# Performance work log

Hardware: AMD Instinct MI355X
Metric: run time of the kernel (lower is better)

Reference implementation:

```python
import jax, jax.numpy as jnp
import numpy as np

NUM_SRC = 100000
NUM_DST = 100000
NNZ = 3200000  # 100k nodes * avg degree 32
BATCH = 64


def setup_inputs() -> dict:
    key = jax.random.key(0)
    k1, k2, k3, k4, k5 = jax.random.split(key, 5)
    row = jax.random.randint(k1, (NNZ,), 0, NUM_DST)   # destination index per edge
    col = jax.random.randint(k2, (NNZ,), 0, NUM_SRC)   # source index per edge
    vals = jax.random.normal(k3, (NNZ,), dtype=jnp.float32) * 0.05  # effective weights
    x = jax.random.normal(k4, (BATCH, NUM_SRC), dtype=jnp.float32)
    bias = jax.random.normal(k5, (NUM_DST,), dtype=jnp.float32) * 0.01
    return {"x": x, "vals": vals, "bias": bias, "row": row, "col": col}


def reference(x, vals, bias, row, col):
    # COO SpMM: out[b, d] = sum_{e: row[e]==d} vals[e] * x[b, col[e]]  (+ bias[d])
    # Equivalent to torch.sparse.mm(sp, x.T).T + bias with sp (num_dst, num_src).
    num_dst = bias.shape[0]
    xt = x.T                                   # (num_src, B)
    contrib = vals[:, None] * xt[col]          # (nnz, B) gather + scale
    out = jax.ops.segment_sum(contrib, row, num_segments=num_dst)  # (num_dst, B)
    return out.T + bias[None, :]               # (B, num_dst)
```

## Files before the change

kernel.cpp:

```cpp
#include <hip/hip_runtime.h>
#include <hip/hip_fp16.h>


#define BSHIFT 7
#define BSIZE 128
#define MAXB 1024
#define TILE 8192
#define EPT 8
#define BINCAP 4992
#define SCAP 4672
#define OVFCAP (1 << 20)

__global__ __launch_bounds__(1024) void transpose_x_kernel(
    const float* __restrict__ x, __half* __restrict__ xTh, int nsrc) {
  __shared__ float tile[64][65];
  int s0 = blockIdx.x * 64;
  int tx = threadIdx.x;
  int ty = threadIdx.y;
#pragma unroll
  for (int i = 0; i < 4; ++i) {
    int b = ty + i * 16;
    int s = s0 + tx;
    tile[tx][b] = (s < nsrc) ? x[(size_t)b * nsrc + s] : 0.f;
  }
  __syncthreads();
#pragma unroll
  for (int i = 0; i < 4; ++i) {
    int sl = ty + i * 16;
    int s = s0 + sl;
    if (s < nsrc) xTh[(size_t)s * 64 + tx] = __float2half(tile[sl][tx]);
  }
}

__global__ __launch_bounds__(1024) void bin_scatter_kernel(
    const int* __restrict__ row, const int* __restrict__ col,
    const float* __restrict__ vals, int* __restrict__ cursor,
    int2* __restrict__ gpk, int2* __restrict__ ovfA, float* __restrict__ ovfB,
    int* __restrict__ ovfCnt, int nnz, int nbins) {
  __shared__ int cnt[MAXB];
  __shared__ int tb[MAXB];
  const int t0 = blockIdx.x * TILE;
  for (int j = threadIdx.x; j < nbins; j += 1024) cnt[j] = 0;
  __syncthreads();
  int rank[EPT];
#pragma unroll
  for (int k = 0; k < EPT; ++k) {
    int e = t0 + k * 1024 + threadIdx.x;
    if (e < nnz) rank[k] = atomicAdd(&cnt[row[e] >> BSHIFT], 1);
  }
  __syncthreads();
  for (int j = threadIdx.x; j < nbins; j += 1024) {
    int n = cnt[j];
    tb[j] = n ? atomicAdd(&cursor[j], n) : 0;
  }
  __syncthreads();
#pragma unroll
  for (int k = 0; k < EPT; ++k) {
    int e = t0 + k * 1024 + threadIdx.x;
    if (e < nnz) {
      int r = row[e], c = col[e];
      float v = vals[e];
      int b = r >> BSHIFT;
      int pos = tb[b] + rank[k];
      if (pos < BINCAP) {
        gpk[(size_t)b * BINCAP + pos] =
            make_int2((c << BSHIFT) | (r & (BSIZE - 1)), __float_as_int(v));
      } else {
        int oi = atomicAdd(ovfCnt, 1);
        if (oi < OVFCAP) {
          ovfA[oi] = make_int2(c, r);
          ovfB[oi] = v;
        }
      }
    }
  }
}

__global__ __launch_bounds__(512) void fused_spmm_kernel(
    const int2* __restrict__ gpk, const int* __restrict__ cursor,
    const __half* __restrict__ xTh, const float* __restrict__ bias,
    float* __restrict__ out, int2* __restrict__ ovfA, float* __restrict__ ovfB,
    int* __restrict__ ovfCnt, int ndst) {
  __shared__ int2 sedge[SCAP];
  __shared__ int cnt[BSIZE];
  __shared__ int exc[BSIZE];
  __shared__ int rk[BSIZE];
  const int b = blockIdx.x;
  const int t = threadIdx.x;
  int cur = cursor[b];
  const int n = (cur < BINCAP) ? cur : BINCAP;
  const int2* bg = gpk + (size_t)b * BINCAP;
  const int d0 = b << BSHIFT;
  if (t < BSIZE) {
    cnt[t] = 0;
    rk[t] = 0;
  }
  __syncthreads();
  for (int e = t; e < n; e += 512) atomicAdd(&cnt[bg[e].x & (BSIZE - 1)], 1);
  __syncthreads();
  if (t < BSIZE) exc[t] = cnt[t];
  __syncthreads();
#pragma unroll
  for (int o = 1; o < BSIZE; o <<= 1) {
    int v = (t >= o && t < BSIZE) ? exc[t - o] : 0;
    __syncthreads();
    if (t < BSIZE) exc[t] += v;
    __syncthreads();
  }
  if (t < BSIZE) exc[t] -= cnt[t];
  __syncthreads();
  for (int e = t; e < n; e += 512) {
    int2 p = bg[e];
    int dl = p.x & (BSIZE - 1);
    int pos = exc[dl] + atomicAdd(&rk[dl], 1);
    if (pos < SCAP) {
      sedge[pos] = p;
    } else {
      int oi = atomicAdd(ovfCnt, 1);
      if (oi < OVFCAP) {
        ovfA[oi] = make_int2(p.x >> BSHIFT, d0 + dl);
        ovfB[oi] = __int_as_float(p.y);
      }
    }
  }
  __syncthreads();
  const int lane = t & 63;
  const int w = t >> 6;
  float accq[16];
#pragma unroll
  for (int q = 0; q < 16; ++q) {
    const int dl = w + (q << 3);
    const int s = exc[dl];
    int e2 = s + cnt[dl];
    if (e2 > SCAP) e2 = SCAP;
    float acc = 0.f;
    int j = s;
    for (; j + 8 <= e2; j += 8) {
      int2 p[8];
#pragma unroll
      for (int k = 0; k < 8; ++k) p[k] = sedge[j + k];
      float xv[8];
#pragma unroll
      for (int k = 0; k < 8; ++k)
        xv[k] = __half2float(xTh[((size_t)(p[k].x >> BSHIFT) << 6) + lane]);
#pragma unroll
      for (int k = 0; k < 8; ++k) acc = fmaf(__int_as_float(p[k].y), xv[k], acc);
    }
    for (; j < e2; ++j) {
      int2 p = sedge[j];
      acc = fmaf(__int_as_float(p.y),
                 __half2float(xTh[((size_t)(p.x >> BSHIFT) << 6) + lane]), acc);
    }
    accq[q] = acc;
  }
  __syncthreads();
  float* tr = (float*)sedge;
#pragma unroll
  for (int q = 0; q < 16; ++q) {
    const int dl = w + (q << 3);
    tr[dl * 65 + lane] = accq[q];
  }
  __syncthreads();
  for (int i = t; i < BSIZE * 64; i += 512) {
    int dl = i & (BSIZE - 1);
    int br = i >> BSHIFT;
    int d = d0 + dl;
    if (d < ndst) out[(size_t)br * ndst + d] = tr[dl * 65 + br] + bias[d];
  }
}

__global__ __launch_bounds__(256) void ovf_fix_kernel(
    const int2* __restrict__ ovfA, const float* __restrict__ ovfB,
    const int* __restrict__ ovfCnt, const __half* __restrict__ xTh,
    float* __restrict__ out, int ndst) {
  int n = *ovfCnt;
  if (n > OVFCAP) n = OVFCAP;
  const int lane = threadIdx.x & 63;
  const int w = threadIdx.x >> 6;
  for (int i = w; i < n; i += 4) {
    int2 cd = ovfA[i];
    float v = ovfB[i];
    float xv = __half2float(xTh[((size_t)cd.x << 6) + lane]);
    unsafeAtomicAdd(&out[(size_t)lane * ndst + cd.y], v * xv);
  }
}

extern "C" void kernel_launch(void* const* d_in, const int* in_sizes, int n_in,
                              void* d_out, int out_size, void* d_ws, size_t ws_size,
                              hipStream_t stream) {
  const float* x = (const float*)d_in[0];
  const float* vals = (const float*)d_in[1];
  const float* bias = (const float*)d_in[2];
  const int* row = (const int*)d_in[3];
  const int* col = (const int*)d_in[4];
  float* out = (float*)d_out;

  const int nnz = in_sizes[1];
  const int ndst = in_sizes[2];
  const int B = out_size / ndst;
  const int nsrc = in_sizes[0] / B;
  const int nbins = (ndst + BSIZE - 1) >> BSHIFT;

  size_t off = 0;
  auto take = [&](size_t bytes) {
    void* p = (char*)d_ws + off;
    off += (bytes + 255) & ~(size_t)255;
    return p;
  };
  __half* xTh = (__half*)take((size_t)nsrc * 64 * 2);
  int2* gpk = (int2*)take((size_t)nbins * BINCAP * 8);
  int2* ovfA = (int2*)take((size_t)OVFCAP * 8);
  float* ovfB = (float*)take((size_t)OVFCAP * 4);
  int* cursor = (int*)take((size_t)nbins * 4);
  int* ovfCnt = (int*)take(256);
  (void)ws_size;

  hipMemsetAsync(cursor, 0, (size_t)nbins * 4, stream);
  hipMemsetAsync(ovfCnt, 0, 4, stream);

  {
    dim3 blk(64, 16);
    int grid = (nsrc + 63) / 64;
    transpose_x_kernel<<<grid, blk, 0, stream>>>(x, xTh, nsrc);
  }
  {
    int grid = (nnz + TILE - 1) / TILE;
    bin_scatter_kernel<<<grid, 1024, 0, stream>>>(row, col, vals, cursor, gpk,
                                                  ovfA, ovfB, ovfCnt, nnz,
                                                  nbins);
  }
  fused_spmm_kernel<<<nbins, 512, 0, stream>>>(gpk, cursor, xTh, bias, out,
                                               ovfA, ovfB, ovfCnt, ndst);
  ovf_fix_kernel<<<1, 256, 0, stream>>>(ovfA, ovfB, ovfCnt, xTh, out, ndst);
}
```

Baseline: 145.4 us.

## Split each destination bin across two SpMM blocks, halving per-block shared memory

Each 128-row bin is now handled by two blocks, each owning 64 destination rows. Each block filters the bin's edges by half, and the shared edge buffer, counters and accumulators shrink to match. This doubles the grid and is meant to raise occupancy and spread load, since per-block LDS drops from about 37KB to about 19KB. The cost is that both blocks read the whole bin from global memory, doubling that read traffic. The smaller SCAP (2432) could also push more edges into the overflow path if a half-bin gets heavy.

```diff
diff --git a/kernel.cpp b/kernel.cpp
--- a/kernel.cpp
+++ b/kernel.cpp
@@ -8,7 +8,7 @@
 #define TILE 8192
 #define EPT 8
 #define BINCAP 4992
-#define SCAP 4672
+#define SCAP 2432
 #define OVFCAP (1 << 20)
 
 __global__ __launch_bounds__(1024) void transpose_x_kernel(
@@ -82,36 +82,41 @@
     float* __restrict__ out, int2* __restrict__ ovfA, float* __restrict__ ovfB,
     int* __restrict__ ovfCnt, int ndst) {
   __shared__ int2 sedge[SCAP];
-  __shared__ int cnt[BSIZE];
-  __shared__ int exc[BSIZE];
-  __shared__ int rk[BSIZE];
-  const int b = blockIdx.x;
+  __shared__ int cnt[64];
+  __shared__ int exc[64];
+  __shared__ int rk[64];
+  const int cb = blockIdx.x >> 1;
+  const int h = blockIdx.x & 1;
   const int t = threadIdx.x;
-  int cur = cursor[b];
+  int cur = cursor[cb];
   const int n = (cur < BINCAP) ? cur : BINCAP;
-  const int2* bg = gpk + (size_t)b * BINCAP;
-  const int d0 = b << BSHIFT;
-  if (t < BSIZE) {
+  const int2* bg = gpk + (size_t)cb * BINCAP;
+  const int d0 = (cb << BSHIFT) + (h << 6);
+  if (t < 64) {
     cnt[t] = 0;
     rk[t] = 0;
   }
   __syncthreads();
-  for (int e = t; e < n; e += 512) atomicAdd(&cnt[bg[e].x & (BSIZE - 1)], 1);
-  __syncthreads();
-  if (t < BSIZE) exc[t] = cnt[t];
-  __syncthreads();
-#pragma unroll
-  for (int o = 1; o < BSIZE; o <<= 1) {
-    int v = (t >= o && t < BSIZE) ? exc[t - o] : 0;
+  for (int e = t; e < n; e += 512) {
+    int pk = bg[e].x;
+    if (((pk >> 6) & 1) == h) atomicAdd(&cnt[pk & 63], 1);
+  }
+  __syncthreads();
+  if (t < 64) exc[t] = cnt[t];
+  __syncthreads();
+#pragma unroll
+  for (int o = 1; o < 64; o <<= 1) {
+    int v = (t >= o && t < 64) ? exc[t - o] : 0;
     __syncthreads();
-    if (t < BSIZE) exc[t] += v;
+    if (t < 64) exc[t] += v;
     __syncthreads();
   }
-  if (t < BSIZE) exc[t] -= cnt[t];
+  if (t < 64) exc[t] -= cnt[t];
   __syncthreads();
   for (int e = t; e < n; e += 512) {
     int2 p = bg[e];
-    int dl = p.x & (BSIZE - 1);
+    if (((p.x >> 6) & 1) != h) continue;
+    int dl = p.x & 63;
     int pos = exc[dl] + atomicAdd(&rk[dl], 1);
     if (pos < SCAP) {
       sedge[pos] = p;
@@ -126,9 +131,9 @@
   __syncthreads();
   const int lane = t & 63;
   const int w = t >> 6;
-  float accq[16];
-#pragma unroll
-  for (int q = 0; q < 16; ++q) {
+  float accq[8];
+#pragma unroll
+  for (int q = 0; q < 8; ++q) {
     const int dl = w + (q << 3);
     const int s = exc[dl];
     int e2 = s + cnt[dl];
@@ -156,14 +161,14 @@
   __syncthreads();
   float* tr = (float*)sedge;
 #pragma unroll
-  for (int q = 0; q < 16; ++q) {
+  for (int q = 0; q < 8; ++q) {
     const int dl = w + (q << 3);
     tr[dl * 65 + lane] = accq[q];
   }
   __syncthreads();
-  for (int i = t; i < BSIZE * 64; i += 512) {
-    int dl = i & (BSIZE - 1);
-    int br = i >> BSHIFT;
+  for (int i = t; i < 64 * 64; i += 512) {
+    int dl = i & 63;
+    int br = i >> 6;
     int d = d0 + dl;
     if (d < ndst) out[(size_t)br * ndst + d] = tr[dl * 65 + br] + bias[d];
   }
@@ -229,7 +234,7 @@
                                                   ovfA, ovfB, ovfCnt, nnz,
                                                   nbins);
   }
-  fused_spmm_kernel<<<nbins, 512, 0, stream>>>(gpk, cursor, xTh, bias, out,
-                                               ovfA, ovfB, ovfCnt, ndst);
+  fused_spmm_kernel<<<2 * nbins, 512, 0, stream>>>(gpk, cursor, xTh, bias, out,
+                                                   ovfA, ovfB, ovfCnt, ndst);
   ovf_fix_kernel<<<1, 256, 0, stream>>>(ovfA, ovfB, ovfCnt, xTh, out, ndst);
 }
```

After: 149.9 us. 1.03x slower.

## Merge x transpose and edge binning into one heterogeneous prep kernel

Applied to the files above, without the earlier changes.

Fuses the x transpose/fp16 conversion kernel and the COO bin-scatter kernel into a single launch, with block index choosing the role, so the two independent stages can run concurrently. It also doubles edges per scatter block to cut global cursor atomics, and merges the two memsets into one contiguous memset. Larger tiles reduce scatter parallelism and raise register use from the rank array, and the shared tile now adds to every block's LDS footprint.

```diff
diff --git a/kernel.cpp b/kernel.cpp
--- a/kernel.cpp
+++ b/kernel.cpp
@@ -5,73 +5,73 @@
 #define BSHIFT 7
 #define BSIZE 128
 #define MAXB 1024
-#define TILE 8192
-#define EPT 8
+#define TILE 16384
+#define EPT 16
 #define BINCAP 4992
 #define SCAP 4672
 #define OVFCAP (1 << 20)
 
-__global__ __launch_bounds__(1024) void transpose_x_kernel(
-    const float* __restrict__ x, __half* __restrict__ xTh, int nsrc) {
-  __shared__ float tile[64][65];
-  int s0 = blockIdx.x * 64;
-  int tx = threadIdx.x;
-  int ty = threadIdx.y;
-#pragma unroll
-  for (int i = 0; i < 4; ++i) {
-    int b = ty + i * 16;
-    int s = s0 + tx;
-    tile[tx][b] = (s < nsrc) ? x[(size_t)b * nsrc + s] : 0.f;
-  }
-  __syncthreads();
-#pragma unroll
-  for (int i = 0; i < 4; ++i) {
-    int sl = ty + i * 16;
-    int s = s0 + sl;
-    if (s < nsrc) xTh[(size_t)s * 64 + tx] = __float2half(tile[sl][tx]);
-  }
-}
-
-__global__ __launch_bounds__(1024) void bin_scatter_kernel(
+__global__ __launch_bounds__(1024) void prep_kernel(
+    const float* __restrict__ x, __half* __restrict__ xTh,
     const int* __restrict__ row, const int* __restrict__ col,
     const float* __restrict__ vals, int* __restrict__ cursor,
     int2* __restrict__ gpk, int2* __restrict__ ovfA, float* __restrict__ ovfB,
-    int* __restrict__ ovfCnt, int nnz, int nbins) {
+    int* __restrict__ ovfCnt, int nnz, int nbins, int nsrc, int nsb) {
   __shared__ int cnt[MAXB];
   __shared__ int tb[MAXB];
-  const int t0 = blockIdx.x * TILE;
-  for (int j = threadIdx.x; j < nbins; j += 1024) cnt[j] = 0;
-  __syncthreads();
-  int rank[EPT];
-#pragma unroll
-  for (int k = 0; k < EPT; ++k) {
-    int e = t0 + k * 1024 + threadIdx.x;
-    if (e < nnz) rank[k] = atomicAdd(&cnt[row[e] >> BSHIFT], 1);
-  }
-  __syncthreads();
-  for (int j = threadIdx.x; j < nbins; j += 1024) {
-    int n = cnt[j];
-    tb[j] = n ? atomicAdd(&cursor[j], n) : 0;
-  }
-  __syncthreads();
-#pragma unroll
-  for (int k = 0; k < EPT; ++k) {
-    int e = t0 + k * 1024 + threadIdx.x;
-    if (e < nnz) {
-      int r = row[e], c = col[e];
-      float v = vals[e];
-      int b = r >> BSHIFT;
-      int pos = tb[b] + rank[k];
-      if (pos < BINCAP) {
-        gpk[(size_t)b * BINCAP + pos] =
-            make_int2((c << BSHIFT) | (r & (BSIZE - 1)), __float_as_int(v));
-      } else {
-        int oi = atomicAdd(ovfCnt, 1);
-        if (oi < OVFCAP) {
-          ovfA[oi] = make_int2(c, r);
-          ovfB[oi] = v;
+  __shared__ float tile[64][65];
+  if (blockIdx.x < nsb) {
+    const int t0 = blockIdx.x * TILE;
+    for (int j = threadIdx.x; j < nbins; j += 1024) cnt[j] = 0;
+    __syncthreads();
+    int rank[EPT];
+#pragma unroll
+    for (int k = 0; k < EPT; ++k) {
+      int e = t0 + k * 1024 + threadIdx.x;
+      if (e < nnz) rank[k] = atomicAdd(&cnt[row[e] >> BSHIFT], 1);
+    }
+    __syncthreads();
+    for (int j = threadIdx.x; j < nbins; j += 1024) {
+      int n = cnt[j];
+      tb[j] = n ? atomicAdd(&cursor[j], n) : 0;
+    }
+    __syncthreads();
+#pragma unroll
+    for (int k = 0; k < EPT; ++k) {
+      int e = t0 + k * 1024 + threadIdx.x;
+      if (e < nnz) {
+        int r = row[e], c = col[e];
+        float v = vals[e];
+        int b = r >> BSHIFT;
+        int pos = tb[b] + rank[k];
+        if (pos < BINCAP) {
+          gpk[(size_t)b * BINCAP + pos] =
+              make_int2((c << BSHIFT) | (r & (BSIZE - 1)), __float_as_int(v));
+        } else {
+          int oi = atomicAdd(ovfCnt, 1);
+          if (oi < OVFCAP) {
+            ovfA[oi] = make_int2(c, r);
+            ovfB[oi] = v;
+          }
         }
       }
+    }
+  } else {
+    int s0 = (blockIdx.x - nsb) * 64;
+    int tx = threadIdx.x & 63;
+    int ty = threadIdx.x >> 6;
+#pragma unroll
+    for (int i = 0; i < 4; ++i) {
+      int b = ty + i * 16;
+      int s = s0 + tx;
+      tile[tx][b] = (s < nsrc) ? x[(size_t)b * nsrc + s] : 0.f;
+    }
+    __syncthreads();
+#pragma unroll
+    for (int i = 0; i < 4; ++i) {
+      int sl = ty + i * 16;
+      int s = s0 + sl;
+      if (s < nsrc) xTh[(size_t)s * 64 + tx] = __float2half(tile[sl][tx]);
     }
   }
 }
@@ -211,23 +211,19 @@
   int2* gpk = (int2*)take((size_t)nbins * BINCAP * 8);
   int2* ovfA = (int2*)take((size_t)OVFCAP * 8);
   float* ovfB = (float*)take((size_t)OVFCAP * 4);
-  int* cursor = (int*)take((size_t)nbins * 4);
-  int* ovfCnt = (int*)take(256);
+  int* meta = (int*)take((size_t)(nbins + 64) * 4);
+  int* cursor = meta;
+  int* ovfCnt = meta + nbins;
   (void)ws_size;
 
-  hipMemsetAsync(cursor, 0, (size_t)nbins * 4, stream);
-  hipMemsetAsync(ovfCnt, 0, 4, stream);
+  hipMemsetAsync(meta, 0, (size_t)(nbins + 1) * 4, stream);
 
   {
-    dim3 blk(64, 16);
-    int grid = (nsrc + 63) / 64;
-    transpose_x_kernel<<<grid, blk, 0, stream>>>(x, xTh, nsrc);
-  }
-  {
-    int grid = (nnz + TILE - 1) / TILE;
-    bin_scatter_kernel<<<grid, 1024, 0, stream>>>(row, col, vals, cursor, gpk,
-                                                  ovfA, ovfB, ovfCnt, nnz,
-                                                  nbins);
+    int nsb = (nnz + TILE - 1) / TILE;
+    int ntb = (nsrc + 63) / 64;
+    prep_kernel<<<nsb + ntb, 1024, 0, stream>>>(x, xTh, row, col, vals, cursor,
+                                                gpk, ovfA, ovfB, ovfCnt, nnz,
+                                                nbins, nsrc, nsb);
   }
   fused_spmm_kernel<<<nbins, 512, 0, stream>>>(gpk, cursor, xTh, bias, out,
                                                ovfA, ovfB, ovfCnt, ndst);
```

Result: faster. 129.5 us, median of 2 (-11.0%).
